# Optimization experiments

Hardware: AMD Instinct MI355X
Metric: run time of the kernel (lower is better)

Reference implementation:

```python
import jax, jax.numpy as jnp
import numpy as np

WIN = 8
NUM_HEADS = 4
DIM = 128


def _relative_position_index(ws):
    coords = np.stack(np.meshgrid(np.arange(ws), np.arange(ws), indexing='ij'))  # (2, ws, ws)
    cf = coords.reshape(2, -1)                      # (2, ws*ws)
    rel = (cf[:, :, None] - cf[:, None, :]).transpose(1, 2, 0).astype(np.int64)  # (N, N, 2)
    rel[..., 0] += ws - 1
    rel[..., 1] += ws - 1
    rel[..., 0] *= 2 * ws - 1
    return rel.sum(-1)                              # (N, N) int64


def setup_inputs() -> dict:
    key = jax.random.key(0)
    ks = jax.random.split(key, 8)
    B_, N, C = 4096, WIN * WIN, DIM
    nW = 4096
    x = jax.random.normal(ks[0], (B_, N, C), dtype=jnp.float32)
    mask = jax.random.normal(ks[1], (nW, N, N), dtype=jnp.float32)
    wq = jax.random.normal(ks[2], (C, C), dtype=jnp.float32) * 0.02
    bq = jnp.zeros((C,), dtype=jnp.float32)
    wkv = jax.random.normal(ks[3], (2 * C, C), dtype=jnp.float32) * 0.02
    bkv = jnp.zeros((2 * C,), dtype=jnp.float32)
    bias_table = jax.random.normal(ks[4], ((2 * WIN - 1) * (2 * WIN - 1), NUM_HEADS), dtype=jnp.float32) * 0.02
    wproj = jax.random.normal(ks[5], (C, C), dtype=jnp.float32) * 0.02
    bproj = jnp.zeros((C,), dtype=jnp.float32)
    rel_index = jnp.asarray(_relative_position_index(WIN))
    return {"x": x, "wq": wq, "bq": bq, "wkv": wkv, "bkv": bkv,
            "bias_table": bias_table, "wproj": wproj, "bproj": bproj,
            "mask": mask, "rel_index": rel_index}


def reference(x, wq, bq, wkv, bkv, bias_table, wproj, bproj, mask, rel_index):
    B_, N, C = x.shape
    H = NUM_HEADS
    d = C // H
    scale = d ** -0.5
    # qkv projection (attn_kv=None path)
    q = (x @ wq.T + bq).reshape(B_, N, H, d).transpose(0, 2, 1, 3)      # (B_, H, N, d)
    kv = (x @ wkv.T + bkv).reshape(B_, N, 2, H, d)
    k = kv[:, :, 0].transpose(0, 2, 1, 3)                               # (B_, H, N, d)
    v = kv[:, :, 1].transpose(0, 2, 1, 3)
    attn = jnp.einsum('bhnd,bhmd->bhnm', q * scale, k)                  # (B_, H, N, N)
    # relative position bias gather: (N*N,) -> (N, N, H) -> (H, N, N)
    rpb = bias_table[rel_index.reshape(-1)].reshape(N, N, H).transpose(2, 0, 1)
    attn = attn + rpb[None]
    # shifted-window mask: attn viewed as (B_//nW, nW, H, N, N) + mask (nW, 1, N, N)
    nW = mask.shape[0]
    attn = (attn.reshape(B_ // nW, nW, H, N, N) + mask[None, :, None]).reshape(B_, H, N, N)
    attn = jax.nn.softmax(attn, axis=-1)
    out = jnp.einsum('bhnm,bhmd->bhnd', attn, v).transpose(0, 2, 1, 3).reshape(B_, N, C)
    return out @ wproj.T + bproj
```

## Files before the change

kernel.cpp:

```cpp
#include <hip/hip_runtime.h>


typedef __bf16 bf16x8 __attribute__((ext_vector_type(8)));
typedef __bf16 bf16x4 __attribute__((ext_vector_type(4)));
typedef float f32x4 __attribute__((ext_vector_type(4)));

#define LOG2E 1.4426950408889634f
#define QSCALE (0.17677669529663687f * 1.4426950408889634f)

__global__ __launch_bounds__(256)
void prep_kernel(const float* __restrict__ wq,
                 const float* __restrict__ wkv,
                 const float* __restrict__ wp,
                 const float* __restrict__ bt,
                 const int* __restrict__ ri,
                 char* __restrict__ ws) {
  int t = blockIdx.x * 256 + (int)threadIdx.x;
  if (t < 8192) {
    int s = t >> 11;
    int c = t & 2047;
    int lane = c & 63, kk = (c >> 6) & 3, ct = c >> 8;
    int li = lane & 15, q4 = lane >> 4;
    int col = ct * 16 + li;
    int ko = kk * 32 + q4 * 8;
    const float* src = (s == 0) ? (wq + col * 128 + ko)
                     : (s == 1) ? (wkv + col * 128 + ko)
                     : (s == 2) ? (wkv + (col + 128) * 128 + ko)
                                : (wp + col * 128 + ko);
    bf16x8 v;
#pragma unroll
    for (int i = 0; i < 8; ++i) v[i] = (__bf16)src[i];
    *(bf16x8*)(ws + s * 32768 + c * 16) = v;
  } else {
    int c = t - 8192;
    int lane = c & 63, tj = (c >> 6) & 3, ti = (c >> 8) & 3, h = (c >> 10) & 3;
    int li = lane & 15, q4 = lane >> 4;
    int m = tj * 16 + li;
    f32x4 r;
#pragma unroll
    for (int rr = 0; rr < 4; ++rr) {
      int n = ti * 16 + q4 * 4 + rr;
      r[rr] = LOG2E * bt[ri[n * 64 + m] * 4 + h];
    }
    *(f32x4*)(ws + 131072 + c * 16) = r;
  }
}

static __device__ __forceinline__ bf16x8 cvt8(const float* __restrict__ p) {
  bf16x8 r;
#pragma unroll
  for (int i = 0; i < 8; ++i) r[i] = (__bf16)p[i];
  return r;
}

static __device__ __forceinline__ int xaddr(int r, int c) {
  return (r << 8) + ((((c >> 3) ^ (r & 7)) << 4)) + ((c & 7) << 1);
}
static __device__ __forceinline__ int qaddr(int r, int c) {
  return (r << 6) + ((((c >> 3) ^ ((r >> 2) & 3)) << 4)) + ((c & 7) << 1);
}
static __device__ __forceinline__ int paddr(int r, int c) {
  return (r << 7) + ((((c >> 3) ^ (r & 7)) << 4)) + ((c & 7) << 1);
}
static __device__ __forceinline__ int vtaddr(int dd, int m) {
  return (dd << 7) + ((((m >> 3) ^ (dd & 7)) << 4)) + ((m & 7) << 1);
}

#define MFMA16(acc, afr, bfr) \
  acc = __builtin_amdgcn_mfma_f32_16x16x32_bf16(afr, bfr, acc, 0, 0, 0)

__global__ __launch_bounds__(256, 2)
void winattn_kernel(const float* __restrict__ xg,
                    const float* __restrict__ bq,
                    const float* __restrict__ bkv,
                    const float* __restrict__ bp,
                    const float* __restrict__ mask,
                    const char* __restrict__ ws,
                    float* __restrict__ out) {
  __shared__ char smem[65536];
  const int b = blockIdx.x;
  const int tid = (int)threadIdx.x;
  const int h = tid >> 6;
  const int lane = tid & 63;
  const int q4 = lane >> 4;
  const int li = lane & 15;
  const int Wb = 16384 + h * 12288;
  const int Qb = Wb, Kb = Wb + 4096, Pb = Wb, Vb = Wb + 8192;
  const bf16x8* __restrict__ wqP = (const bf16x8*)(ws);
  const bf16x8* __restrict__ wkP = (const bf16x8*)(ws + 32768);
  const bf16x8* __restrict__ wvP = (const bf16x8*)(ws + 65536);
  const bf16x8* __restrict__ wpP = (const bf16x8*)(ws + 98304);
  const f32x4* __restrict__ rpbP = (const f32x4*)(ws + 131072);

  {
    const float* xw = xg + b * 8192;
#pragma unroll
    for (int rep = 0; rep < 4; ++rep) {
      int chunk = rep * 256 + tid;
      int r = chunk >> 4, cc = chunk & 15;
      bf16x8 v = cvt8(xw + r * 128 + cc * 8);
      *(bf16x8*)(smem + xaddr(r, cc * 8)) = v;
    }
  }
  __syncthreads();

  {
    f32x4 aq[4][2] = {}; f32x4 ak[4][2] = {}; f32x4 av[4][2] = {};
#pragma unroll
    for (int kk = 0; kk < 4; ++kk) {
      bf16x8 a[4];
#pragma unroll
      for (int ti = 0; ti < 4; ++ti)
        a[ti] = *(const bf16x8*)(smem + xaddr(ti * 16 + li, kk * 32 + q4 * 8));
#pragma unroll
      for (int tj = 0; tj < 2; ++tj) {
        int wi = ((h * 2 + tj) * 4 + kk) * 64 + lane;
        bf16x8 wbq = wqP[wi];
        bf16x8 wbk = wkP[wi];
        bf16x8 wbv = wvP[wi];
#pragma unroll
        for (int ti = 0; ti < 4; ++ti) {
          MFMA16(aq[ti][tj], a[ti], wbq);
          MFMA16(ak[ti][tj], a[ti], wbk);
          MFMA16(av[ti][tj], a[ti], wbv);
        }
      }
    }
#pragma unroll
    for (int tj = 0; tj < 2; ++tj) {
      int col = h * 32 + tj * 16 + li;
      float bqv = bq[col];
      float bkk = bkv[col];
      float bvv = bkv[col + 128];
      int lc = tj * 16 + li;
#pragma unroll
      for (int ti = 0; ti < 4; ++ti) {
        __bf16 qs[4], ks[4], vs[4];
#pragma unroll
        for (int rr = 0; rr < 4; ++rr) {
          qs[rr] = (__bf16)((aq[ti][tj][rr] + bqv) * QSCALE);
          ks[rr] = (__bf16)(ak[ti][tj][rr] + bkk);
          vs[rr] = (__bf16)(av[ti][tj][rr] + bvv);
        }
#pragma unroll
        for (int rr = 0; rr < 4; ++rr) {
          int row = ti * 16 + q4 * 4 + rr;
          *(__bf16*)(smem + Qb + qaddr(row, lc)) = qs[rr];
          *(__bf16*)(smem + Kb + qaddr(row, lc)) = ks[rr];
        }
        int m0 = ti * 16 + q4 * 4;
        bf16x4 vv = { vs[0], vs[1], vs[2], vs[3] };
        *(bf16x4*)(smem + Vb + vtaddr(lc, m0)) = vv;
      }
    }
  }
  asm volatile("s_waitcnt lgkmcnt(0)" ::: "memory");

  float bias[4][4][4];
  {
    const float* mw = mask + b * 4096;
#pragma unroll
    for (int ti = 0; ti < 4; ++ti)
#pragma unroll
      for (int tj = 0; tj < 4; ++tj) {
        f32x4 rv = rpbP[((h * 4 + ti) * 4 + tj) * 64 + lane];
        int m = tj * 16 + li;
#pragma unroll
        for (int rr = 0; rr < 4; ++rr) {
          int n = ti * 16 + q4 * 4 + rr;
          bias[ti][tj][rr] = fmaf(LOG2E, mw[n * 64 + m], rv[rr]);
        }
      }
  }

  f32x4 S[4][4];
  {
    bf16x8 qf[4], kf[4];
#pragma unroll
    for (int t = 0; t < 4; ++t) {
      qf[t] = *(const bf16x8*)(smem + Qb + qaddr(t * 16 + li, q4 * 8));
      kf[t] = *(const bf16x8*)(smem + Kb + qaddr(t * 16 + li, q4 * 8));
    }
#pragma unroll
    for (int ti = 0; ti < 4; ++ti)
#pragma unroll
      for (int tj = 0; tj < 4; ++tj) {
        f32x4 c = { bias[ti][tj][0], bias[ti][tj][1],
                    bias[ti][tj][2], bias[ti][tj][3] };
        S[ti][tj] = __builtin_amdgcn_mfma_f32_16x16x32_bf16(qf[ti], kf[tj], c, 0, 0, 0);
      }
  }

  float rinv[4][4];
#pragma unroll
  for (int ti = 0; ti < 4; ++ti)
#pragma unroll
    for (int rr = 0; rr < 4; ++rr) {
      float mx = fmaxf(fmaxf(S[ti][0][rr], S[ti][1][rr]),
                       fmaxf(S[ti][2][rr], S[ti][3][rr]));
      mx = fmaxf(mx, __shfl_xor(mx, 1));
      mx = fmaxf(mx, __shfl_xor(mx, 2));
      mx = fmaxf(mx, __shfl_xor(mx, 4));
      mx = fmaxf(mx, __shfl_xor(mx, 8));
      float s = 0.f;
#pragma unroll
      for (int tj = 0; tj < 4; ++tj) {
        float e = __builtin_amdgcn_exp2f(S[ti][tj][rr] - mx);
        S[ti][tj][rr] = e;
        s += e;
      }
      s += __shfl_xor(s, 1);
      s += __shfl_xor(s, 2);
      s += __shfl_xor(s, 4);
      s += __shfl_xor(s, 8);
      rinv[ti][rr] = __builtin_amdgcn_rcpf(s);
    }

#pragma unroll
  for (int ti = 0; ti < 4; ++ti)
#pragma unroll
    for (int rr = 0; rr < 4; ++rr) {
      int n = ti * 16 + q4 * 4 + rr;
#pragma unroll
      for (int tj = 0; tj < 4; ++tj) {
        int m = tj * 16 + li;
        *(__bf16*)(smem + Pb + paddr(n, m)) = (__bf16)S[ti][tj][rr];
      }
    }
  asm volatile("s_waitcnt lgkmcnt(0)" ::: "memory");

  f32x4 O[4][2] = {};
#pragma unroll
  for (int ks = 0; ks < 2; ++ks) {
    bf16x8 pf[4], vf[2];
#pragma unroll
    for (int ti = 0; ti < 4; ++ti)
      pf[ti] = *(const bf16x8*)(smem + Pb + paddr(ti * 16 + li, ks * 32 + q4 * 8));
#pragma unroll
    for (int tj = 0; tj < 2; ++tj)
      vf[tj] = *(const bf16x8*)(smem + Vb + vtaddr(tj * 16 + li, ks * 32 + q4 * 8));
#pragma unroll
    for (int ti = 0; ti < 4; ++ti)
#pragma unroll
      for (int tj = 0; tj < 2; ++tj)
        MFMA16(O[ti][tj], pf[ti], vf[tj]);
  }

  __syncthreads();
#pragma unroll
  for (int ti = 0; ti < 4; ++ti)
#pragma unroll
    for (int tj = 0; tj < 2; ++tj)
#pragma unroll
      for (int rr = 0; rr < 4; ++rr) {
        int row = ti * 16 + q4 * 4 + rr;
        int col = h * 32 + tj * 16 + li;
        *(__bf16*)(smem + xaddr(row, col)) = (__bf16)(O[ti][tj][rr] * rinv[ti][rr]);
      }
  __syncthreads();

  {
    f32x4 acc[4][2] = {};
#pragma unroll
    for (int kk = 0; kk < 4; ++kk) {
      bf16x8 a[4];
#pragma unroll
      for (int ti = 0; ti < 4; ++ti)
        a[ti] = *(const bf16x8*)(smem + xaddr(ti * 16 + li, kk * 32 + q4 * 8));
#pragma unroll
      for (int tj = 0; tj < 2; ++tj) {
        int wi = ((h * 2 + tj) * 4 + kk) * 64 + lane;
        bf16x8 wb = wpP[wi];
#pragma unroll
        for (int ti = 0; ti < 4; ++ti)
          MFMA16(acc[ti][tj], a[ti], wb);
      }
    }
    float* ow = out + b * 8192;
#pragma unroll
    for (int tj = 0; tj < 2; ++tj) {
      int col = h * 32 + tj * 16 + li;
      float bpv = bp[col];
#pragma unroll
      for (int ti = 0; ti < 4; ++ti)
#pragma unroll
        for (int rr = 0; rr < 4; ++rr) {
          int row = ti * 16 + q4 * 4 + rr;
          ow[row * 128 + col] = acc[ti][tj][rr] + bpv;
        }
    }
  }
}

extern "C" void kernel_launch(void* const* d_in, const int* in_sizes, int n_in,
                              void* d_out, int out_size, void* d_ws, size_t ws_size,
                              hipStream_t stream) {
  (void)in_sizes; (void)n_in; (void)ws_size; (void)out_size;
  prep_kernel<<<96, 256, 0, stream>>>(
      (const float*)d_in[1],
      (const float*)d_in[3],
      (const float*)d_in[6],
      (const float*)d_in[5],
      (const int*)d_in[9],
      (char*)d_ws);
  winattn_kernel<<<4096, 256, 0, stream>>>(
      (const float*)d_in[0],
      (const float*)d_in[2],
      (const float*)d_in[4],
      (const float*)d_in[7],
      (const float*)d_in[8],
      (const char*)d_ws,
      (float*)d_out);
}
```

Baseline: 336.4 us.

## Compute transposed Q/K tiles for vector stores and shrink LDS for three blocks per CU

Q and K projections are now computed transposed (weights as the A operand), so each lane holds four consecutive feature values and can write them as one bf16x4 store instead of four scalar stores. V is moved into the x staging region after a block barrier, which cuts shared memory from 64 KB to 48 KB per block. The launch bound is raised to allow three resident blocks per CU. The price is an extra __syncthreads and a tighter register budget, which could cause spills.

```diff
diff --git a/kernel.cpp b/kernel.cpp
--- a/kernel.cpp
+++ b/kernel.cpp
@@ -69,7 +69,7 @@
 #define MFMA16(acc, afr, bfr) \
   acc = __builtin_amdgcn_mfma_f32_16x16x32_bf16(afr, bfr, acc, 0, 0, 0)
 
-__global__ __launch_bounds__(256, 2)
+__global__ __launch_bounds__(256, 3)
 void winattn_kernel(const float* __restrict__ xg,
                     const float* __restrict__ bq,
                     const float* __restrict__ bkv,
@@ -77,15 +77,16 @@
                     const float* __restrict__ mask,
                     const char* __restrict__ ws,
                     float* __restrict__ out) {
-  __shared__ char smem[65536];
+  __shared__ char smem[49152];
   const int b = blockIdx.x;
   const int tid = (int)threadIdx.x;
   const int h = tid >> 6;
   const int lane = tid & 63;
   const int q4 = lane >> 4;
   const int li = lane & 15;
-  const int Wb = 16384 + h * 12288;
-  const int Qb = Wb, Kb = Wb + 4096, Pb = Wb, Vb = Wb + 8192;
+  const int Wb = 16384 + h * 8192;
+  const int Qb = Wb, Kb = Wb + 4096, Pb = Wb;
+  const int Vb = h * 4096;
   const bf16x8* __restrict__ wqP = (const bf16x8*)(ws);
   const bf16x8* __restrict__ wkP = (const bf16x8*)(ws + 32768);
   const bf16x8* __restrict__ wvP = (const bf16x8*)(ws + 65536);
@@ -105,52 +106,57 @@
   __syncthreads();
 
   {
-    f32x4 aq[4][2] = {}; f32x4 ak[4][2] = {}; f32x4 av[4][2] = {};
+    f32x4 aqT[2][4] = {}; f32x4 akT[2][4] = {}; f32x4 av[4][2] = {};
 #pragma unroll
     for (int kk = 0; kk < 4; ++kk) {
       bf16x8 a[4];
 #pragma unroll
-      for (int ti = 0; ti < 4; ++ti)
-        a[ti] = *(const bf16x8*)(smem + xaddr(ti * 16 + li, kk * 32 + q4 * 8));
-#pragma unroll
-      for (int tj = 0; tj < 2; ++tj) {
-        int wi = ((h * 2 + tj) * 4 + kk) * 64 + lane;
+      for (int nt = 0; nt < 4; ++nt)
+        a[nt] = *(const bf16x8*)(smem + xaddr(nt * 16 + li, kk * 32 + q4 * 8));
+#pragma unroll
+      for (int mt = 0; mt < 2; ++mt) {
+        int wi = ((h * 2 + mt) * 4 + kk) * 64 + lane;
         bf16x8 wbq = wqP[wi];
         bf16x8 wbk = wkP[wi];
         bf16x8 wbv = wvP[wi];
 #pragma unroll
-        for (int ti = 0; ti < 4; ++ti) {
-          MFMA16(aq[ti][tj], a[ti], wbq);
-          MFMA16(ak[ti][tj], a[ti], wbk);
-          MFMA16(av[ti][tj], a[ti], wbv);
+        for (int nt = 0; nt < 4; ++nt) {
+          MFMA16(aqT[mt][nt], wbq, a[nt]);
+          MFMA16(akT[mt][nt], wbk, a[nt]);
+          MFMA16(av[nt][mt], a[nt], wbv);
         }
       }
     }
+#pragma unroll
+    for (int mt = 0; mt < 2; ++mt) {
+      f32x4 bq4 = *(const f32x4*)(bq + h * 32 + mt * 16 + q4 * 4);
+      f32x4 bk4 = *(const f32x4*)(bkv + h * 32 + mt * 16 + q4 * 4);
+      int f0 = mt * 16 + q4 * 4;
+#pragma unroll
+      for (int nt = 0; nt < 4; ++nt) {
+        bf16x4 qv, kv;
+#pragma unroll
+        for (int rr = 0; rr < 4; ++rr) {
+          qv[rr] = (__bf16)((aqT[mt][nt][rr] + bq4[rr]) * QSCALE);
+          kv[rr] = (__bf16)(akT[mt][nt][rr] + bk4[rr]);
+        }
+        int row = nt * 16 + li;
+        *(bf16x4*)(smem + Qb + qaddr(row, f0)) = qv;
+        *(bf16x4*)(smem + Kb + qaddr(row, f0)) = kv;
+      }
+    }
+    __syncthreads();
 #pragma unroll
     for (int tj = 0; tj < 2; ++tj) {
       int col = h * 32 + tj * 16 + li;
-      float bqv = bq[col];
-      float bkk = bkv[col];
       float bvv = bkv[col + 128];
       int lc = tj * 16 + li;
 #pragma unroll
       for (int ti = 0; ti < 4; ++ti) {
-        __bf16 qs[4], ks[4], vs[4];
-#pragma unroll
-        for (int rr = 0; rr < 4; ++rr) {
-          qs[rr] = (__bf16)((aq[ti][tj][rr] + bqv) * QSCALE);
-          ks[rr] = (__bf16)(ak[ti][tj][rr] + bkk);
-          vs[rr] = (__bf16)(av[ti][tj][rr] + bvv);
-        }
-#pragma unroll
-        for (int rr = 0; rr < 4; ++rr) {
-          int row = ti * 16 + q4 * 4 + rr;
-          *(__bf16*)(smem + Qb + qaddr(row, lc)) = qs[rr];
-          *(__bf16*)(smem + Kb + qaddr(row, lc)) = ks[rr];
-        }
-        int m0 = ti * 16 + q4 * 4;
-        bf16x4 vv = { vs[0], vs[1], vs[2], vs[3] };
-        *(bf16x4*)(smem + Vb + vtaddr(lc, m0)) = vv;
+        bf16x4 vv;
+#pragma unroll
+        for (int rr = 0; rr < 4; ++rr) vv[rr] = (__bf16)(av[ti][tj][rr] + bvv);
+        *(bf16x4*)(smem + Vb + vtaddr(lc, ti * 16 + q4 * 4)) = vv;
       }
     }
   }
```

Result: slower. 347.2 us (+3.2%).
